# Performance work log

Measured on AMD Instinct MI355X. Metric: run time of the kernel, lower is better.

Reference implementation:

```python
import jax, jax.numpy as jnp
import numpy as np


def _xavier_uniform(key, shape):
    # torch xavier_uniform_ on 4D: receptive = prod(shape[2:]),
    # fan_in = shape[1]*receptive, fan_out = shape[0]*receptive
    receptive = int(np.prod(shape[2:]))
    fan_in = shape[1] * receptive
    fan_out = shape[0] * receptive
    bound = float(np.sqrt(6.0 / (fan_in + fan_out)))
    return jax.random.uniform(key, shape, jnp.float32, -bound, bound)


def setup_inputs() -> dict:
    key = jax.random.key(0)
    k1, k2, k3, k4 = jax.random.split(key, 4)
    B, m, H, Hk, vk, D = 128, 64, 64, 64, 16, 16  # note: source bug requires m == H
    return {
        "x_0": jax.random.normal(k1, (B, m, D), jnp.float32),
        "x_h": jax.random.normal(k2, (B, H, D), jnp.float32),  # values unused by the original forward (bug)
        "Vm": _xavier_uniform(k3, (Hk, 1, m, vk)),
        "Vh": _xavier_uniform(k4, (Hk, 1, vk, H)),
    }


def reference(x_0, x_h, Vm, Vh):
    # Faithful to the torch source, including its bug: x_h is recomputed from x_0.
    # Original math: x_k[b,d,i,j] = x0r[b,d,i] * xhr[b,d,j];
    #   out[b,k,d] = sum_{i,j} x_k[b,d,i,j] * (Vm @ Vh)[k,i,j]
    # Reassociated via the rank-vk factorization to avoid the [B,Hk,D,m,H] intermediate.
    B, m, D = x_0.shape
    H = x_h.shape[1]
    x0r = jnp.transpose(x_0, (0, 2, 1))      # [B, D, m]
    # source: transpose twice with .contiguous() then reshape -> flat reinterpretation of x_0
    xhr = x_0.reshape(B, D, H)               # [B, D, H]  (requires m == H)
    a = jnp.einsum('bdi,kiv->bkdv', x0r, Vm[:, 0])   # [B, Hk, D, vk]
    b = jnp.einsum('bdj,kvj->bkdv', xhr, Vh[:, 0])   # [B, Hk, D, vk]
    return jnp.einsum('bkdv,bkdv->bkd', a, b)        # [B, Hk, D]
```

## Files before the change

### kernel.cpp

```cpp
#include <hip/hip_runtime.h>
#include <stdint.h>


typedef __attribute__((ext_vector_type(8))) short bf8;
typedef __attribute__((ext_vector_type(4))) float f4;

#define NM 64
#define ND 16
#define NK 64
#define NV 16

__device__ __forceinline__ unsigned short f2bf(float f) {
    union { float f; unsigned u; } x; x.f = f;
    return (unsigned short)((x.u + 0x8000u) >> 16);
}

template <bool FP32>
__device__ __forceinline__ bf8 gatherFrag(const void* p, int base) {
    bf8 r;
    if (FP32) {
        const float* q = (const float*)p + base;
#pragma unroll
        for (int e = 0; e < 8; ++e) r[e] = (short)f2bf(q[e * 16]);
    } else {
        const unsigned short* q = (const unsigned short*)p + base;
#pragma unroll
        for (int e = 0; e < 8; ++e) r[e] = (short)q[e * 16];
    }
    return r;
}

template <bool FP32>
__device__ __forceinline__ bf8 contigFrag(const void* p, int base) {
    bf8 r;
    if (FP32) {
        const f4* q = (const f4*)((const float*)p + base);
        f4 lo = q[0], hi = q[1];
#pragma unroll
        for (int e = 0; e < 4; ++e) {
            r[e]     = (short)f2bf(lo[e]);
            r[e + 4] = (short)f2bf(hi[e]);
        }
    } else {
        r = *(const bf8*)((const unsigned short*)p + base);
    }
    return r;
}

template <bool FP32>
__device__ __forceinline__ void run(const void* __restrict__ x0,
                                    const void* __restrict__ vm,
                                    const void* __restrict__ vh,
                                    void* __restrict__ out) {
    const int l      = threadIdx.x;
    const int lane16 = l & 15;
    const int quad   = l >> 4;
    const int b      = blockIdx.x >> 4;
    const int kg     = blockIdx.x & 15;

    const int xb = b * (NM * ND);

    bf8 a1[2], a2[2];
#pragma unroll
    for (int s = 0; s < 2; ++s) {
        a1[s] = gatherFrag<FP32>(x0, xb + (s * 32 + quad * 8) * 16 + lane16);
        a2[s] = contigFrag<FP32>(x0, xb + lane16 * 64 + s * 32 + quad * 8);
    }

#pragma unroll
    for (int kk = 0; kk < 4; ++kk) {
        const int k  = kg * 4 + kk;
        const int wb = k * (NM * NV);

        bf8 b1[2], b2[2];
#pragma unroll
        for (int s = 0; s < 2; ++s) {
            b1[s] = gatherFrag<FP32>(vm, wb + (s * 32 + quad * 8) * 16 + lane16);
            b2[s] = contigFrag<FP32>(vh, wb + lane16 * 64 + s * 32 + quad * 8);
        }

        f4 ac = {0.f, 0.f, 0.f, 0.f}, bc = {0.f, 0.f, 0.f, 0.f};
#pragma unroll
        for (int s = 0; s < 2; ++s) {
            ac = __builtin_amdgcn_mfma_f32_16x16x32_bf16(a1[s], b1[s], ac, 0, 0, 0);
            bc = __builtin_amdgcn_mfma_f32_16x16x32_bf16(a2[s], b2[s], bc, 0, 0, 0);
        }

        float p0 = ac[0] * bc[0], p1 = ac[1] * bc[1];
        float p2 = ac[2] * bc[2], p3 = ac[3] * bc[3];
#pragma unroll
        for (int off = 1; off < 16; off <<= 1) {
            p0 += __shfl_xor(p0, off);
            p1 += __shfl_xor(p1, off);
            p2 += __shfl_xor(p2, off);
            p3 += __shfl_xor(p3, off);
        }
        if (lane16 == 0) {
            const int ob = b * (NK * ND) + k * ND + quad * 4;
            if (FP32) {
                f4 w = {p0, p1, p2, p3};
                *(f4*)((float*)out + ob) = w;
            } else {
                ushort4 w;
                w.x = f2bf(p0); w.y = f2bf(p1); w.z = f2bf(p2); w.w = f2bf(p3);
                *(ushort4*)((unsigned short*)out + ob) = w;
            }
        }
    }
}

__global__ void __launch_bounds__(64) cin_kernel(const void* __restrict__ x0,
                                                 const void* __restrict__ vm,
                                                 const void* __restrict__ vh,
                                                 void* __restrict__ out) {
    unsigned u  = ((const unsigned*)x0)[threadIdx.x];
    unsigned ex = (u >> 7) & 0xffu;
    bool inr    = (ex > 100u && ex < 150u);
    bool isbf16 = __popcll(__ballot(inr)) >= 48;
    if (isbf16) run<false>(x0, vm, vh, out);
    else        run<true>(x0, vm, vh, out);
}

extern "C" void kernel_launch(void* const* d_in, const int* in_sizes, int n_in,
                              void* d_out, int out_size, void* d_ws, size_t ws_size,
                              hipStream_t stream) {
    const int nb = in_sizes[0] / (NM * ND);
    cin_kernel<<<dim3(nb * 16), dim3(64), 0, stream>>>(
        d_in[0], d_in[2], d_in[3], d_out);
}
```

Baseline: 65.05 us.

## Pre-convert inputs to bf16 fragment layout in a prep kernel, widen blocks

Adds a prep kernel that converts x0, Vm and Vh to bf16 and writes them into a workspace in the layout the MFMA fragments need, so the main kernel can load contiguous 16-byte fragments instead of strided scalar gathers with per-element conversion. The main kernel now runs 4 waves per 256-thread block, each wave covering a group of k values. The cost is a second launch plus an extra global round trip through the workspace. The workspace indexing mapping must exactly match the old fragment layouts.

Measured after the change: 66.39 us. 2.1% more time.

```diff
diff --git a/kernel.cpp b/kernel.cpp
--- a/kernel.cpp
+++ b/kernel.cpp
@@ -15,76 +15,90 @@
     return (unsigned short)((x.u + 0x8000u) >> 16);
 }
 
-template <bool FP32>
-__device__ __forceinline__ bf8 gatherFrag(const void* p, int base) {
-    bf8 r;
-    if (FP32) {
-        const float* q = (const float*)p + base;
-#pragma unroll
-        for (int e = 0; e < 8; ++e) r[e] = (short)f2bf(q[e * 16]);
-    } else {
-        const unsigned short* q = (const unsigned short*)p + base;
-#pragma unroll
-        for (int e = 0; e < 8; ++e) r[e] = (short)q[e * 16];
-    }
-    return r;
+__device__ __forceinline__ bool senseBF16(const void* x0) {
+    unsigned u  = ((const unsigned*)x0)[threadIdx.x & 63];
+    unsigned ex = (u >> 7) & 0xffu;
+    bool inr    = (ex > 100u && ex < 150u);
+    return __popcll(__ballot(inr)) >= 48;
 }
 
 template <bool FP32>
-__device__ __forceinline__ bf8 contigFrag(const void* p, int base) {
-    bf8 r;
-    if (FP32) {
-        const f4* q = (const f4*)((const float*)p + base);
-        f4 lo = q[0], hi = q[1];
-#pragma unroll
-        for (int e = 0; e < 4; ++e) {
-            r[e]     = (short)f2bf(lo[e]);
-            r[e + 4] = (short)f2bf(hi[e]);
-        }
+__device__ __forceinline__ void prep_body(const void* __restrict__ x0,
+                                          const void* __restrict__ vm,
+                                          const void* __restrict__ vh,
+                                          unsigned short* __restrict__ ws,
+                                          int t, int nx0, int nvm) {
+    const void* p;
+    int src;
+    if (t < nx0) {
+        int b = t >> 10, rem = t & 1023, d = rem >> 6, i = rem & 63;
+        src = b * 1024 + i * 16 + d;  p = x0;
+    } else if (t < 2 * nx0) {
+        src = t - nx0;  p = x0;
+    } else if (t < 2 * nx0 + nvm) {
+        int s = t - 2 * nx0;
+        int k = s >> 10, rem = s & 1023, v = rem >> 6, i = rem & 63;
+        src = k * 1024 + i * 16 + v;  p = vm;
     } else {
-        r = *(const bf8*)((const unsigned short*)p + base);
+        src = t - (2 * nx0 + nvm);  p = vh;
     }
-    return r;
+    unsigned short o;
+    if (FP32) o = f2bf(((const float*)p)[src]);
+    else      o = ((const unsigned short*)p)[src];
+    ws[t] = o;
 }
 
-template <bool FP32>
-__device__ __forceinline__ void run(const void* __restrict__ x0,
-                                    const void* __restrict__ vm,
-                                    const void* __restrict__ vh,
-                                    void* __restrict__ out) {
-    const int l      = threadIdx.x;
+__global__ void __launch_bounds__(256) cin_prep(const void* __restrict__ x0,
+                                                const void* __restrict__ vm,
+                                                const void* __restrict__ vh,
+                                                unsigned short* __restrict__ ws,
+                                                int nx0, int nvm, int total) {
+    int t = blockIdx.x * 256 + threadIdx.x;
+    bool isbf16 = senseBF16(x0);
+    if (t >= total) return;
+    if (isbf16) prep_body<false>(x0, vm, vh, ws, t, nx0, nvm);
+    else        prep_body<true>(x0, vm, vh, ws, t, nx0, nvm);
+}
+
+__global__ void __launch_bounds__(256) cin_main(const unsigned short* __restrict__ ws,
+                                                const void* __restrict__ x0,
+                                                void* __restrict__ out,
+                                                int nx0, int nvm) {
+    const int tid    = threadIdx.x;
+    const int l      = tid & 63;
+    const int w      = tid >> 6;
     const int lane16 = l & 15;
     const int quad   = l >> 4;
-    const int b      = blockIdx.x >> 4;
-    const int kg     = blockIdx.x & 15;
+    const int b      = blockIdx.x >> 2;
+    const int kg     = (blockIdx.x & 3) * 4 + w;
 
-    const int xb = b * (NM * ND);
+    const bool isbf16 = senseBF16(x0);
+
+    const int fi0 = lane16 * 8 + quad;
+    const int fi1 = fi0 + 4;
+
+    const unsigned short* x0t = ws + b * 1024;
+    const unsigned short* x0c = ws + nx0 + b * 1024;
+    const unsigned short* vmt = ws + 2 * nx0;
+    const unsigned short* vhc = ws + 2 * nx0 + nvm;
 
     bf8 a1[2], a2[2];
-#pragma unroll
-    for (int s = 0; s < 2; ++s) {
-        a1[s] = gatherFrag<FP32>(x0, xb + (s * 32 + quad * 8) * 16 + lane16);
-        a2[s] = contigFrag<FP32>(x0, xb + lane16 * 64 + s * 32 + quad * 8);
-    }
+    a1[0] = ((const bf8*)x0t)[fi0];  a1[1] = ((const bf8*)x0t)[fi1];
+    a2[0] = ((const bf8*)x0c)[fi0];  a2[1] = ((const bf8*)x0c)[fi1];
 
 #pragma unroll
     for (int kk = 0; kk < 4; ++kk) {
-        const int k  = kg * 4 + kk;
-        const int wb = k * (NM * NV);
-
-        bf8 b1[2], b2[2];
-#pragma unroll
-        for (int s = 0; s < 2; ++s) {
-            b1[s] = gatherFrag<FP32>(vm, wb + (s * 32 + quad * 8) * 16 + lane16);
-            b2[s] = contigFrag<FP32>(vh, wb + lane16 * 64 + s * 32 + quad * 8);
-        }
+        const int k = kg * 4 + kk;
+        const bf8* b1p = (const bf8*)(vmt + k * 1024);
+        const bf8* b2p = (const bf8*)(vhc + k * 1024);
+        bf8 b1_0 = b1p[fi0], b1_1 = b1p[fi1];
+        bf8 b2_0 = b2p[fi0], b2_1 = b2p[fi1];
 
         f4 ac = {0.f, 0.f, 0.f, 0.f}, bc = {0.f, 0.f, 0.f, 0.f};
-#pragma unroll
-        for (int s = 0; s < 2; ++s) {
-            ac = __builtin_amdgcn_mfma_f32_16x16x32_bf16(a1[s], b1[s], ac, 0, 0, 0);
-            bc = __builtin_amdgcn_mfma_f32_16x16x32_bf16(a2[s], b2[s], bc, 0, 0, 0);
-        }
+        ac = __builtin_amdgcn_mfma_f32_16x16x32_bf16(a1[0], b1_0, ac, 0, 0, 0);
+        bc = __builtin_amdgcn_mfma_f32_16x16x32_bf16(a2[0], b2_0, bc, 0, 0, 0);
+        ac = __builtin_amdgcn_mfma_f32_16x16x32_bf16(a1[1], b1_1, ac, 0, 0, 0);
+        bc = __builtin_amdgcn_mfma_f32_16x16x32_bf16(a2[1], b2_1, bc, 0, 0, 0);
 
         float p0 = ac[0] * bc[0], p1 = ac[1] * bc[1];
         float p2 = ac[2] * bc[2], p3 = ac[3] * bc[3];
@@ -97,34 +111,30 @@
         }
         if (lane16 == 0) {
             const int ob = b * (NK * ND) + k * ND + quad * 4;
-            if (FP32) {
-                f4 w = {p0, p1, p2, p3};
-                *(f4*)((float*)out + ob) = w;
+            if (isbf16) {
+                ushort4 o;
+                o.x = f2bf(p0); o.y = f2bf(p1); o.z = f2bf(p2); o.w = f2bf(p3);
+                *(ushort4*)((unsigned short*)out + ob) = o;
             } else {
-                ushort4 w;
-                w.x = f2bf(p0); w.y = f2bf(p1); w.z = f2bf(p2); w.w = f2bf(p3);
-                *(ushort4*)((unsigned short*)out + ob) = w;
+                f4 o = {p0, p1, p2, p3};
+                *(f4*)((float*)out + ob) = o;
             }
         }
     }
 }
 
-__global__ void __launch_bounds__(64) cin_kernel(const void* __restrict__ x0,
-                                                 const void* __restrict__ vm,
-                                                 const void* __restrict__ vh,
-                                                 void* __restrict__ out) {
-    unsigned u  = ((const unsigned*)x0)[threadIdx.x];
-    unsigned ex = (u >> 7) & 0xffu;
-    bool inr    = (ex > 100u && ex < 150u);
-    bool isbf16 = __popcll(__ballot(inr)) >= 48;
-    if (isbf16) run<false>(x0, vm, vh, out);
-    else        run<true>(x0, vm, vh, out);
-}
-
 extern "C" void kernel_launch(void* const* d_in, const int* in_sizes, int n_in,
                               void* d_out, int out_size, void* d_ws, size_t ws_size,
                               hipStream_t stream) {
-    const int nb = in_sizes[0] / (NM * ND);
-    cin_kernel<<<dim3(nb * 16), dim3(64), 0, stream>>>(
-        d_in[0], d_in[2], d_in[3], d_out);
+    const int nx0 = in_sizes[0];
+    const int nvm = in_sizes[2];
+    const int nvh = in_sizes[3];
+    const int nb  = nx0 / (NM * ND);
+    const int total = 2 * nx0 + nvm + nvh;
+
+    unsigned short* ws = (unsigned short*)d_ws;
+    cin_prep<<<dim3((total + 255) / 256), dim3(256), 0, stream>>>(
+        d_in[0], d_in[2], d_in[3], ws, nx0, nvm, total);
+    cin_main<<<dim3(nb * 4), dim3(256), 0, stream>>>(
+        ws, d_in[0], d_out, nx0, nvm);
 }
```
